# Kernel optimization log

Measured on AMD Instinct MI355X. Metric: run time of the kernel, lower is better.

The kernel has to match this reference:

```python
import jax, jax.numpy as jnp
import numpy as np

B, DX, DZ = 262144, 8, 4

def setup_inputs() -> dict:
    key = jax.random.key(0)
    kx, kz, kp, kh = jax.random.split(key, 4)
    x = jax.random.normal(kx, (B, DX, 1), dtype=jnp.float32)
    z = jax.random.normal(kz, (B, DZ, 1), dtype=jnp.float32)
    # P must be SPD so that S = H P H^T + R is invertible
    A = jax.random.normal(kp, (B, DX, DX), dtype=jnp.float32)
    P = jnp.matmul(A, jnp.swapaxes(A, -1, -2)) / DX + jnp.eye(DX, dtype=jnp.float32)
    H = jax.random.normal(kh, (DZ, DX), dtype=jnp.float32)
    R = jnp.eye(DZ, dtype=jnp.float32)
    return {"x": x, "z": z, "P": P, "H": H, "R": R}

def reference(x, z, P, H, R):
    # Batched Kalman update; per-batch math identical to the torch forward.
    Ix = jnp.eye(DX, dtype=x.dtype)
    y = z - jnp.einsum('zx,bxo->bzo', H, x)                  # innovation [B,DZ,1]
    PHT = jnp.einsum('bxy,zy->bxz', P, H)                    # P H^T      [B,DX,DZ]
    S = jnp.einsum('zx,bxw->bzw', H, PHT) + R                # H P H^T + R [B,DZ,DZ]
    SI = jnp.linalg.inv(S)
    K = jnp.matmul(PHT, SI)                                  # Kalman gain [B,DX,DZ]
    x_new = x + jnp.matmul(K, y)                             # [B,DX,1]
    I_KH = Ix - jnp.einsum('bxz,zy->bxy', K, H)              # [B,DX,DX]
    P_new = (jnp.matmul(jnp.matmul(I_KH, P), jnp.swapaxes(I_KH, -1, -2))
             + jnp.matmul(jnp.einsum('bxz,zw->bxw', K, R), jnp.swapaxes(K, -1, -2)))
    # torch: cat((x.T, P)) -> [1+DX, DX]; batched -> [B, 1+DX, DX]
    return jnp.concatenate((jnp.swapaxes(x_new, -1, -2), P_new), axis=1)
```

## Files before the change

### kernel.cpp

```cpp
#include <hip/hip_runtime.h>

constexpr int B_N = 262144;
constexpr int DX  = 8;
constexpr int DZ  = 4;

__global__ __launch_bounds__(256) void kalman_update(
    const float* __restrict__ x_in,
    const float* __restrict__ z_in,
    const float* __restrict__ P_in,
    const float* __restrict__ H_in,
    const float* __restrict__ R_in,
    float* __restrict__ out)
{
    const int b = blockIdx.x * 256 + threadIdx.x;
    if (b >= B_N) return;

    float H[DZ][DX];
#pragma unroll
    for (int i = 0; i < DZ * DX; ++i) H[i / DX][i % DX] = H_in[i];
    float R[DZ][DZ];
#pragma unroll
    for (int i = 0; i < DZ * DZ; ++i) R[i / DZ][i % DZ] = R_in[i];

    float x[DX];
    {
        const float4* p = reinterpret_cast<const float4*>(x_in + (size_t)b * DX);
        float4 a = p[0], c = p[1];
        x[0] = a.x; x[1] = a.y; x[2] = a.z; x[3] = a.w;
        x[4] = c.x; x[5] = c.y; x[6] = c.z; x[7] = c.w;
    }
    float y[DZ];
    {
        const float4* p = reinterpret_cast<const float4*>(z_in + (size_t)b * DZ);
        float4 a = p[0];
        y[0] = a.x; y[1] = a.y; y[2] = a.z; y[3] = a.w;
    }
    float P[DX][DX];
    {
        const float4* p = reinterpret_cast<const float4*>(P_in + (size_t)b * DX * DX);
#pragma unroll
        for (int i = 0; i < 16; ++i) {
            float4 a = p[i];
            const int r = i >> 1, c = (i & 1) * 4;
            P[r][c + 0] = a.x; P[r][c + 1] = a.y; P[r][c + 2] = a.z; P[r][c + 3] = a.w;
        }
    }

#pragma unroll
    for (int zi = 0; zi < DZ; ++zi) {
        float acc = 0.f;
#pragma unroll
        for (int k = 0; k < DX; ++k) acc += H[zi][k] * x[k];
        y[zi] -= acc;
    }

    float PHT[DX][DZ];
#pragma unroll
    for (int i = 0; i < DX; ++i)
#pragma unroll
        for (int j = 0; j < DZ; ++j) {
            float acc = 0.f;
#pragma unroll
            for (int k = 0; k < DX; ++k) acc += P[i][k] * H[j][k];
            PHT[i][j] = acc;
        }

    float S[DZ][DZ];
#pragma unroll
    for (int a = 0; a < DZ; ++a)
#pragma unroll
        for (int c = 0; c < DZ; ++c) {
            float acc = R[a][c];
#pragma unroll
            for (int k = 0; k < DX; ++k) acc += H[a][k] * PHT[k][c];
            S[a][c] = acc;
        }

    float SI[DZ][DZ];
    {
        const float A2323 = S[2][2]*S[3][3] - S[2][3]*S[3][2];
        const float A1323 = S[2][1]*S[3][3] - S[2][3]*S[3][1];
        const float A1223 = S[2][1]*S[3][2] - S[2][2]*S[3][1];
        const float A0323 = S[2][0]*S[3][3] - S[2][3]*S[3][0];
        const float A0223 = S[2][0]*S[3][2] - S[2][2]*S[3][0];
        const float A0123 = S[2][0]*S[3][1] - S[2][1]*S[3][0];
        const float A2313 = S[1][2]*S[3][3] - S[1][3]*S[3][2];
        const float A1313 = S[1][1]*S[3][3] - S[1][3]*S[3][1];
        const float A1213 = S[1][1]*S[3][2] - S[1][2]*S[3][1];
        const float A2312 = S[1][2]*S[2][3] - S[1][3]*S[2][2];
        const float A1312 = S[1][1]*S[2][3] - S[1][3]*S[2][1];
        const float A1212 = S[1][1]*S[2][2] - S[1][2]*S[2][1];
        const float A0313 = S[1][0]*S[3][3] - S[1][3]*S[3][0];
        const float A0213 = S[1][0]*S[3][2] - S[1][2]*S[3][0];
        const float A0312 = S[1][0]*S[2][3] - S[1][3]*S[2][0];
        const float A0212 = S[1][0]*S[2][2] - S[1][2]*S[2][0];
        const float A0113 = S[1][0]*S[3][1] - S[1][1]*S[3][0];
        const float A0112 = S[1][0]*S[2][1] - S[1][1]*S[2][0];

        float det = S[0][0] * (S[1][1]*A2323 - S[1][2]*A1323 + S[1][3]*A1223)
                  - S[0][1] * (S[1][0]*A2323 - S[1][2]*A0323 + S[1][3]*A0223)
                  + S[0][2] * (S[1][0]*A1323 - S[1][1]*A0323 + S[1][3]*A0123)
                  - S[0][3] * (S[1][0]*A1223 - S[1][1]*A0223 + S[1][2]*A0123);
        const float id = 1.0f / det;

        SI[0][0] = id *  (S[1][1]*A2323 - S[1][2]*A1323 + S[1][3]*A1223);
        SI[0][1] = id * -(S[0][1]*A2323 - S[0][2]*A1323 + S[0][3]*A1223);
        SI[0][2] = id *  (S[0][1]*A2313 - S[0][2]*A1313 + S[0][3]*A1213);
        SI[0][3] = id * -(S[0][1]*A2312 - S[0][2]*A1312 + S[0][3]*A1212);
        SI[1][0] = id * -(S[1][0]*A2323 - S[1][2]*A0323 + S[1][3]*A0223);
        SI[1][1] = id *  (S[0][0]*A2323 - S[0][2]*A0323 + S[0][3]*A0223);
        SI[1][2] = id * -(S[0][0]*A2313 - S[0][2]*A0313 + S[0][3]*A0213);
        SI[1][3] = id *  (S[0][0]*A2312 - S[0][2]*A0312 + S[0][3]*A0212);
        SI[2][0] = id *  (S[1][0]*A1323 - S[1][1]*A0323 + S[1][3]*A0123);
        SI[2][1] = id * -(S[0][0]*A1323 - S[0][1]*A0323 + S[0][3]*A0123);
        SI[2][2] = id *  (S[0][0]*A1313 - S[0][1]*A0313 + S[0][3]*A0113);
        SI[2][3] = id * -(S[0][0]*A1312 - S[0][1]*A0312 + S[0][3]*A0112);
        SI[3][0] = id * -(S[1][0]*A1223 - S[1][1]*A0223 + S[1][2]*A0123);
        SI[3][1] = id *  (S[0][0]*A1223 - S[0][1]*A0223 + S[0][2]*A0123);
        SI[3][2] = id * -(S[0][0]*A1213 - S[0][1]*A0213 + S[0][2]*A0113);
        SI[3][3] = id *  (S[0][0]*A1212 - S[0][1]*A0212 + S[0][2]*A0112);
    }

    float K[DX][DZ];
#pragma unroll
    for (int i = 0; i < DX; ++i)
#pragma unroll
        for (int j = 0; j < DZ; ++j) {
            float acc = 0.f;
#pragma unroll
            for (int w = 0; w < DZ; ++w) acc += PHT[i][w] * SI[w][j];
            K[i][j] = acc;
        }

    {
        float xn[DX];
#pragma unroll
        for (int i = 0; i < DX; ++i) {
            float acc = x[i];
#pragma unroll
            for (int zi = 0; zi < DZ; ++zi) acc += K[i][zi] * y[zi];
            xn[i] = acc;
        }
        float4* o = reinterpret_cast<float4*>(out + (size_t)b * 72);
        o[0] = make_float4(xn[0], xn[1], xn[2], xn[3]);
        o[1] = make_float4(xn[4], xn[5], xn[6], xn[7]);
    }

#pragma unroll
    for (int i = 0; i < DX; ++i)
#pragma unroll
        for (int j = 0; j < DX; ++j) {
            float acc = P[i][j];
#pragma unroll
            for (int zi = 0; zi < DZ; ++zi) acc -= K[i][zi] * PHT[j][zi];
            P[i][j] = acc;
        }

    float E[DX][DZ];
#pragma unroll
    for (int i = 0; i < DX; ++i)
#pragma unroll
        for (int zi = 0; zi < DZ; ++zi) {
            float acc = 0.f;
#pragma unroll
            for (int w = 0; w < DZ; ++w) acc += K[i][w] * R[w][zi];
#pragma unroll
            for (int k = 0; k < DX; ++k) acc -= P[i][k] * H[zi][k];
            E[i][zi] = acc;
        }

#pragma unroll
    for (int i = 0; i < DX; ++i) {
#pragma unroll
        for (int j = 0; j < DX; ++j) {
            float acc = P[i][j];
#pragma unroll
            for (int zi = 0; zi < DZ; ++zi) acc += E[i][zi] * K[j][zi];
            P[i][j] = acc;
        }
        float4* o = reinterpret_cast<float4*>(out + (size_t)b * 72 + 8 + (size_t)i * 8);
        o[0] = make_float4(P[i][0], P[i][1], P[i][2], P[i][3]);
        o[1] = make_float4(P[i][4], P[i][5], P[i][6], P[i][7]);
    }
}

extern "C" void kernel_launch(void* const* d_in, const int* in_sizes, int n_in,
                              void* d_out, int out_size, void* d_ws, size_t ws_size,
                              hipStream_t stream) {
    const float* x = (const float*)d_in[0];
    const float* z = (const float*)d_in[1];
    const float* P = (const float*)d_in[2];
    const float* H = (const float*)d_in[3];
    const float* R = (const float*)d_in[4];
    float* out = (float*)d_out;

    dim3 grid(B_N / 256), block(256);
    hipLaunchKernelGGL(kalman_update, grid, block, 0, stream, x, z, P, H, R, out);
}
```

Baseline: 158.0 us.

## Stage per-wave P, x and output through swizzled LDS for coalesced global access

Each wave cooperatively loads its 64 batches' P and x into a per-wave shared-memory slice with contiguous lane-strided float4 loads. Each thread then reads its own matrix from that slice. The outputs are written back to the slice and stored to global memory in a fully coalesced pattern. XOR swizzles are meant to reduce LDS bank conflicts. This replaces the old per-thread 256-byte strided accesses, which coalesced poorly. The cost is roughly 72 KB of LDS per block, which limits blocks per CU, and the kernel relies on intra-wave ordering with no explicit barrier.

New measurement: 145.8 us. 7.7% less time.

```diff
diff --git a/kernel.cpp b/kernel.cpp
--- a/kernel.cpp
+++ b/kernel.cpp
@@ -3,6 +3,10 @@
 constexpr int B_N = 262144;
 constexpr int DX  = 8;
 constexpr int DZ  = 4;
+
+__device__ __forceinline__ int swzP(int i) { return i ^ ((i >> 4) & 7); }
+__device__ __forceinline__ int swzX(int i) { return i ^ ((i >> 3) & 1); }
+__device__ __forceinline__ int swzO(int i) { return i ^ ((i >> 3) & 1); }
 
 __global__ __launch_bounds__(256) void kalman_update(
     const float* __restrict__ x_in,
@@ -12,8 +16,35 @@
     const float* __restrict__ R_in,
     float* __restrict__ out)
 {
-    const int b = blockIdx.x * 256 + threadIdx.x;
-    if (b >= B_N) return;
+    __shared__ float4 lds[4 * 1152];
+
+    const int wave = threadIdx.x >> 6;
+    const int lane = threadIdx.x & 63;
+    float4* const slice = lds + wave * 1152;
+
+    const int wbatch = blockIdx.x * 256 + wave * 64;
+    const int b      = wbatch + lane;
+
+    {
+        const float4* Pg = reinterpret_cast<const float4*>(P_in) + (size_t)wbatch * 16;
+#pragma unroll
+        for (int k = 0; k < 16; ++k) {
+            const int d = 64 * k + lane;
+            slice[swzP(d)] = Pg[d];
+        }
+        const float4* xg = reinterpret_cast<const float4*>(x_in) + (size_t)wbatch * 2;
+#pragma unroll
+        for (int k = 0; k < 2; ++k) {
+            const int d = 64 * k + lane;
+            slice[1024 + swzX(d)] = xg[d];
+        }
+    }
+
+    float y[DZ];
+    {
+        const float4 a = reinterpret_cast<const float4*>(z_in)[b];
+        y[0] = a.x; y[1] = a.y; y[2] = a.z; y[3] = a.w;
+    }
 
     float H[DZ][DX];
 #pragma unroll
@@ -24,26 +55,17 @@
 
     float x[DX];
     {
-        const float4* p = reinterpret_cast<const float4*>(x_in + (size_t)b * DX);
-        float4 a = p[0], c = p[1];
+        const float4 a = slice[1024 + swzX(2 * lane + 0)];
+        const float4 c = slice[1024 + swzX(2 * lane + 1)];
         x[0] = a.x; x[1] = a.y; x[2] = a.z; x[3] = a.w;
         x[4] = c.x; x[5] = c.y; x[6] = c.z; x[7] = c.w;
     }
-    float y[DZ];
-    {
-        const float4* p = reinterpret_cast<const float4*>(z_in + (size_t)b * DZ);
-        float4 a = p[0];
-        y[0] = a.x; y[1] = a.y; y[2] = a.z; y[3] = a.w;
-    }
     float P[DX][DX];
-    {
-        const float4* p = reinterpret_cast<const float4*>(P_in + (size_t)b * DX * DX);
-#pragma unroll
-        for (int i = 0; i < 16; ++i) {
-            float4 a = p[i];
-            const int r = i >> 1, c = (i & 1) * 4;
-            P[r][c + 0] = a.x; P[r][c + 1] = a.y; P[r][c + 2] = a.z; P[r][c + 3] = a.w;
-        }
+#pragma unroll
+    for (int c16 = 0; c16 < 16; ++c16) {
+        const float4 v = slice[swzP(16 * lane + c16)];
+        const int r = c16 >> 1, c = (c16 & 1) * 4;
+        P[r][c + 0] = v.x; P[r][c + 1] = v.y; P[r][c + 2] = v.z; P[r][c + 3] = v.w;
     }
 
 #pragma unroll
@@ -141,9 +163,8 @@
             for (int zi = 0; zi < DZ; ++zi) acc += K[i][zi] * y[zi];
             xn[i] = acc;
         }
-        float4* o = reinterpret_cast<float4*>(out + (size_t)b * 72);
-        o[0] = make_float4(xn[0], xn[1], xn[2], xn[3]);
-        o[1] = make_float4(xn[4], xn[5], xn[6], xn[7]);
+        slice[swzO(18 * lane + 0)] = make_float4(xn[0], xn[1], xn[2], xn[3]);
+        slice[swzO(18 * lane + 1)] = make_float4(xn[4], xn[5], xn[6], xn[7]);
     }
 
 #pragma unroll
@@ -178,9 +199,17 @@
             for (int zi = 0; zi < DZ; ++zi) acc += E[i][zi] * K[j][zi];
             P[i][j] = acc;
         }
-        float4* o = reinterpret_cast<float4*>(out + (size_t)b * 72 + 8 + (size_t)i * 8);
-        o[0] = make_float4(P[i][0], P[i][1], P[i][2], P[i][3]);
-        o[1] = make_float4(P[i][4], P[i][5], P[i][6], P[i][7]);
+        slice[swzO(18 * lane + 2 + 2 * i)]     = make_float4(P[i][0], P[i][1], P[i][2], P[i][3]);
+        slice[swzO(18 * lane + 2 + 2 * i + 1)] = make_float4(P[i][4], P[i][5], P[i][6], P[i][7]);
+    }
+
+    {
+        float4* Og = reinterpret_cast<float4*>(out) + (size_t)wbatch * 18;
+#pragma unroll
+        for (int k = 0; k < 18; ++k) {
+            const int d = 64 * k + lane;
+            Og[d] = slice[swzO(d)];
+        }
     }
 }
 
```
